# Optimization experiments

Hardware: AMD Instinct MI355X
Metric: run time of the kernel (lower is better)

## Reference

```python
import jax, jax.numpy as jnp
import numpy as np

NODE_DIM = 2
EMB_DIM = 128
SEQ_LEN = 201  # must be odd: depot + N pickups + N deliveries
BATCH = 2048


def _basesin(x, T, fai=0.0):
    return np.sin(2 * np.pi / T * np.abs(np.mod(x, 2 * T) - T) + fai)


def _basecos(x, T, fai=0.0):
    return np.cos(2 * np.pi / T * np.abs(np.mod(x, 2 * T) - T) + fai)


def cyclic_position_encoding_pattern(n_position, emb_dim, mean_pooling=True):
    Td_set = np.linspace(np.power(n_position, 1 / (emb_dim // 2)), n_position,
                         emb_dim // 2, dtype='int')
    x = np.zeros((n_position, emb_dim))
    for i in range(emb_dim):
        Td = Td_set[i // 3 * 3 + 1] if i // 3 * 3 + 1 < emb_dim // 2 else Td_set[-1]
        fai = 0 if i <= emb_dim // 2 else 2 * np.pi * ((-i + emb_dim // 2) / (emb_dim // 2))
        longer = np.arange(0, np.ceil(n_position / Td) * Td, 0.01)
        sel = np.linspace(0, len(longer), n_position, dtype='int', endpoint=False)
        if i % 2 == 1:
            x[:, i] = _basecos(longer, Td, fai)[sel]
        else:
            x[:, i] = _basesin(longer, Td, fai)[sel]
    pattern = x.astype(np.float32)
    pattern_sum = np.zeros_like(pattern)
    arange = np.arange(n_position)
    pooling = [-2, -1, 0, 1, 2] if mean_pooling else [0]
    for i in pooling:
        pattern_sum += pattern[(arange + i + n_position) % n_position]
    pattern = pattern_sum / len(pooling) - pattern.mean(0, keepdims=True)
    return jnp.asarray(pattern)


def setup_inputs() -> dict:
    key = jax.random.key(0)
    kx, kw = jax.random.split(key)
    x = jax.random.normal(kx, (BATCH, SEQ_LEN, NODE_DIM), dtype=jnp.float32)
    # random cyclic permutation per batch: cycle visits all nodes starting at 0
    rng = np.random.default_rng(0)
    r = rng.random((BATCH, SEQ_LEN - 1))
    order = np.concatenate([np.zeros((BATCH, 1), dtype=np.int64),
                            np.argsort(r, axis=1).astype(np.int64) + 1], axis=1)
    nxt = np.roll(order, -1, axis=1)
    sol = np.zeros((BATCH, SEQ_LEN), dtype=np.int64)
    np.put_along_axis(sol, order, nxt, axis=1)
    solutions = jnp.asarray(sol)
    # Linear(node_dim, emb_dim, bias=False), init uniform(-stdv, stdv), stdv=1/sqrt(in)
    stdv = 1.0 / np.sqrt(NODE_DIM)
    W = jax.random.uniform(kw, (EMB_DIM, NODE_DIM), dtype=jnp.float32,
                           minval=-stdv, maxval=stdv)
    pattern = cyclic_position_encoding_pattern(SEQ_LEN, EMB_DIM)
    return {"x": x, "solutions": solutions, "W": W, "pattern": pattern}


def _position_indices(solutions):
    """Pointer-chase over the solution cycle; returns visited_time [B,S] int32
    and top2 [B,S,2] int32 (clac_stacks=True path of the original)."""
    B, S = solutions.shape
    half = S // 2
    arange = jnp.arange(B)
    sol = solutions.astype(jnp.int32)

    visited0 = jnp.zeros((B, S), dtype=jnp.int32)
    pre0 = jnp.zeros((B,), dtype=jnp.int32)
    stacks0 = jnp.full((B, half + 1), -0.01, dtype=jnp.float32).at[:, 0].set(0.0)
    top20 = jnp.zeros((B, S, 2), dtype=jnp.int32)

    def step(carry, i):
        visited, pre, stacks, top2 = carry
        cur = sol[arange, pre]                       # [B] current node
        visited = visited.at[arange, cur].set(i + 1)
        # pickups (0 < cur <= half) push i+1; deliveries (cur > half) pop (-0.01);
        # depot (cur == 0) is a no-op (rewrites stacks[:,0] with itself).
        pos = jnp.where(cur > half, cur - half, cur)
        val = jnp.where(cur == 0, stacks[arange, 0],
                        jnp.where(cur > half, jnp.float32(-0.01),
                                  (i + 1).astype(jnp.float32)))
        stacks = stacks.at[arange, pos].set(val)
        _, idx = jax.lax.top_k(stacks, 2)            # [B,2]
        top2 = top2.at[arange, cur].set(idx.astype(jnp.int32))
        return (visited, cur, stacks, top2), None

    (visited, _, _, top2), _ = jax.lax.scan(
        step, (visited0, pre0, stacks0, top20), jnp.arange(S))
    return visited, top2


def reference(x, solutions, W, pattern):
    visited_time, top2 = _position_indices(solutions)
    S = solutions.shape[1]
    # pos_enc[b, j] = pattern[visited_time[b, j] % S]
    pos_enc = jnp.take(pattern, visited_time % S, axis=0)   # [B,S,D]
    x_embedding = jnp.einsum('bsn,dn->bsd', x, W)           # Linear, no bias
    return x_embedding, pos_enc, visited_time.astype(jnp.int64), top2
```

## Files before the change

kernel.cpp:

```cpp
#include <hip/hip_runtime.h>
#include <stdint.h>

#define B 2048
#define S 201
#define HALF 100
#define D 128
#define BS (B * S)
#define OFF_POS (BS * D)
#define OFF_VT  (2 * OFF_POS)
#define OFF_T2  (OFF_VT + BS)
#define F4B (S * (D / 4))
#define TPB 256

typedef float vf4 __attribute__((ext_vector_type(4)));
typedef float vf2 __attribute__((ext_vector_type(2)));

__global__ __launch_bounds__(TPB, 4) void fused(const float* __restrict__ x,
                                                const int* __restrict__ sol,
                                                const float* __restrict__ W,
                                                const float* __restrict__ pattern,
                                                float* __restrict__ out) {
    __shared__ uint8_t  s_sol[S];
    __shared__ uint8_t  s_vis[S];
    __shared__ uint8_t  s_nx[HALF + 1];
    __shared__ uint8_t  s_pv[HALF + 1];
    __shared__ uint16_t s_t2[S];

    const int tid = threadIdx.x;
    const int b   = blockIdx.x;

    if (tid < 64) {
        for (int j = tid; j < S; j += 64) {
            s_sol[j] = (uint8_t)sol[b * S + j];
            s_vis[j] = 0;
            s_t2[j]  = 0;
        }
        asm volatile("s_waitcnt lgkmcnt(0)" ::: "memory");

        if (tid == 0) {
            int pre = 0;
            int head = 0, second = 1;
            unsigned long long m0 = 0, m1 = 0;

            for (int i = 0; i < S; ++i) {
                int cur = s_sol[pre];
                s_vis[cur] = (uint8_t)(i + 1);
                if (cur != 0) {
                    if (cur <= HALF) {
                        s_nx[cur]  = (uint8_t)head;
                        s_pv[head] = (uint8_t)cur;
                        second = head;
                        head   = cur;
                        if (cur < 64) m0 |= 1ull << cur; else m1 |= 1ull << (cur - 64);
                    } else {
                        int q = cur - HALF;
                        bool in = (q < 64) ? ((m0 >> q) & 1ull)
                                           : ((m1 >> (q - 64)) & 1ull);
                        if (in) {
                            if (q < 64) m0 &= ~(1ull << q); else m1 &= ~(1ull << (q - 64));
                            if (q == head) {
                                head = second;
                                second = (head == 0) ? 1 : (int)s_nx[head];
                            } else if (q == second) {
                                int n2 = s_nx[q];
                                s_nx[head] = (uint8_t)n2;
                                s_pv[n2]   = (uint8_t)head;
                                second = n2;
                            } else {
                                int p = s_pv[q], n2 = s_nx[q];
                                s_nx[p]  = (uint8_t)n2;
                                s_pv[n2] = (uint8_t)p;
                            }
                        }
                    }
                }
                s_t2[cur] = (uint16_t)(head | (second << 8));
                pre = cur;
            }
        }
    } else {
        const int t  = tid - 64;
        const int d4 = t & 31;
        const float4* W4 = (const float4*)W;
        float4 w0 = W4[d4 * 2];
        float4 w1 = W4[d4 * 2 + 1];
        const float2* x2 = (const float2*)x + b * S;
        vf4* o4 = (vf4*)out + b * F4B;
        for (int idx4 = t; idx4 < F4B; idx4 += 192) {
            float2 xv = x2[idx4 >> 5];
            vf4 o;
            o.x = xv.x * w0.x + xv.y * w0.y;
            o.y = xv.x * w0.z + xv.y * w0.w;
            o.z = xv.x * w1.x + xv.y * w1.y;
            o.w = xv.x * w1.z + xv.y * w1.w;
            o4[idx4] = o;
        }
    }
    __syncthreads();

    {
        const vf4* p4 = (const vf4*)pattern;
        vf4* o4 = (vf4*)(out + OFF_POS) + b * F4B;
        for (int idx4 = tid; idx4 < F4B; idx4 += TPB) {
            int vt  = s_vis[idx4 >> 5];
            int row = (vt >= S) ? (vt - S) : vt;
            vf4 v = p4[row * 32 + (idx4 & 31)];
            o4[idx4] = v;
        }
        for (int j = tid; j < S; j += TPB) {
            out[OFF_VT + b * S + j] = (float)s_vis[j];
            int tt = s_t2[j];
            vf2 f2 = { (float)(tt & 255), (float)(tt >> 8) };
            ((vf2*)(out + OFF_T2))[b * S + j] = f2;
        }
    }
}

extern "C" void kernel_launch(void* const* d_in, const int* in_sizes, int n_in,
                              void* d_out, int out_size, void* d_ws, size_t ws_size,
                              hipStream_t stream) {
    const float* x       = (const float*)d_in[0];
    const int*   sol     = (const int*)d_in[1];
    const float* W       = (const float*)d_in[2];
    const float* pattern = (const float*)d_in[3];
    float* out = (float*)d_out;

    hipLaunchKernelGGL(fused, dim3(B), dim3(TPB), 0, stream, x, sol, W, pattern, out);
}
```

Before: 434.1 us.

## Process two batch elements per block with parallel serial chases in two waves

Each block now handles two batch rows, running the serial pointer-chasing stack simulation for both at once in separate wavefronts (lanes 0 and 64), while the other two waves write the linear embedding for both rows. The grid is halved. The aim is to overlap two latency-bound serial chains per block and amortise block launch and setup. The cost is fewer embedding-writing threads per row, a barrier now shared by both rows, and half as many blocks to hide latency.

Result: slower. 454.4 us (+4.7%).

```diff
diff --git a/kernel.cpp b/kernel.cpp
--- a/kernel.cpp
+++ b/kernel.cpp
@@ -11,105 +11,120 @@
 #define OFF_T2  (OFF_VT + BS)
 #define F4B (S * (D / 4))
 #define TPB 256
+#define NBLK (B / 2)
 
 typedef float vf4 __attribute__((ext_vector_type(4)));
 typedef float vf2 __attribute__((ext_vector_type(2)));
+
+__device__ __forceinline__ void chase(const uint8_t* __restrict__ sl,
+                                      uint8_t* __restrict__ vis,
+                                      uint16_t* __restrict__ t2,
+                                      uint8_t* __restrict__ nx,
+                                      uint8_t* __restrict__ pv) {
+    int pre = 0;
+    int head = 0, second = 1;
+    unsigned long long m0 = 0, m1 = 0;
+    for (int i = 0; i < S; ++i) {
+        int cur = sl[pre];
+        vis[cur] = (uint8_t)(i + 1);
+        if (cur != 0) {
+            if (cur <= HALF) {
+                nx[cur]  = (uint8_t)head;
+                pv[head] = (uint8_t)cur;
+                second = head;
+                head   = cur;
+                if (cur < 64) m0 |= 1ull << cur; else m1 |= 1ull << (cur - 64);
+            } else {
+                int q = cur - HALF;
+                bool in = (q < 64) ? ((m0 >> q) & 1ull) : ((m1 >> (q - 64)) & 1ull);
+                if (in) {
+                    if (q < 64) m0 &= ~(1ull << q); else m1 &= ~(1ull << (q - 64));
+                    if (q == head) {
+                        head = second;
+                        second = (head == 0) ? 1 : (int)nx[head];
+                    } else if (q == second) {
+                        int n2 = nx[q];
+                        nx[head] = (uint8_t)n2;
+                        pv[n2]   = (uint8_t)head;
+                        second = n2;
+                    } else {
+                        int p = pv[q], n2 = nx[q];
+                        nx[p]  = (uint8_t)n2;
+                        pv[n2] = (uint8_t)p;
+                    }
+                }
+            }
+        }
+        t2[cur] = (uint16_t)(head | (second << 8));
+        pre = cur;
+    }
+}
 
 __global__ __launch_bounds__(TPB, 4) void fused(const float* __restrict__ x,
                                                 const int* __restrict__ sol,
                                                 const float* __restrict__ W,
                                                 const float* __restrict__ pattern,
                                                 float* __restrict__ out) {
-    __shared__ uint8_t  s_sol[S];
-    __shared__ uint8_t  s_vis[S];
-    __shared__ uint8_t  s_nx[HALF + 1];
-    __shared__ uint8_t  s_pv[HALF + 1];
-    __shared__ uint16_t s_t2[S];
+    __shared__ uint8_t  s_sol[2][S];
+    __shared__ uint8_t  s_vis[2][S];
+    __shared__ uint16_t s_t2 [2][S];
+    __shared__ uint8_t  s_nx [2][HALF + 1];
+    __shared__ uint8_t  s_pv [2][HALF + 1];
 
     const int tid = threadIdx.x;
-    const int b   = blockIdx.x;
+    const int b0  = blockIdx.x;
+    const int b1  = blockIdx.x + NBLK;
 
-    if (tid < 64) {
-        for (int j = tid; j < S; j += 64) {
-            s_sol[j] = (uint8_t)sol[b * S + j];
-            s_vis[j] = 0;
-            s_t2[j]  = 0;
-        }
-        asm volatile("s_waitcnt lgkmcnt(0)" ::: "memory");
+    for (int j = tid; j < S; j += TPB) {
+        s_sol[0][j] = (uint8_t)sol[b0 * S + j];
+        s_sol[1][j] = (uint8_t)sol[b1 * S + j];
+        s_vis[0][j] = 0;  s_vis[1][j] = 0;
+        s_t2 [0][j] = 0;  s_t2 [1][j] = 0;
+    }
+    __syncthreads();
 
-        if (tid == 0) {
-            int pre = 0;
-            int head = 0, second = 1;
-            unsigned long long m0 = 0, m1 = 0;
-
-            for (int i = 0; i < S; ++i) {
-                int cur = s_sol[pre];
-                s_vis[cur] = (uint8_t)(i + 1);
-                if (cur != 0) {
-                    if (cur <= HALF) {
-                        s_nx[cur]  = (uint8_t)head;
-                        s_pv[head] = (uint8_t)cur;
-                        second = head;
-                        head   = cur;
-                        if (cur < 64) m0 |= 1ull << cur; else m1 |= 1ull << (cur - 64);
-                    } else {
-                        int q = cur - HALF;
-                        bool in = (q < 64) ? ((m0 >> q) & 1ull)
-                                           : ((m1 >> (q - 64)) & 1ull);
-                        if (in) {
-                            if (q < 64) m0 &= ~(1ull << q); else m1 &= ~(1ull << (q - 64));
-                            if (q == head) {
-                                head = second;
-                                second = (head == 0) ? 1 : (int)s_nx[head];
-                            } else if (q == second) {
-                                int n2 = s_nx[q];
-                                s_nx[head] = (uint8_t)n2;
-                                s_pv[n2]   = (uint8_t)head;
-                                second = n2;
-                            } else {
-                                int p = s_pv[q], n2 = s_nx[q];
-                                s_nx[p]  = (uint8_t)n2;
-                                s_pv[n2] = (uint8_t)p;
-                            }
-                        }
-                    }
-                }
-                s_t2[cur] = (uint16_t)(head | (second << 8));
-                pre = cur;
-            }
+    if (tid < 128) {
+        if ((tid & 63) == 0) {
+            const int w = tid >> 6;
+            chase(s_sol[w], s_vis[w], s_t2[w], s_nx[w], s_pv[w]);
         }
     } else {
-        const int t  = tid - 64;
+        const int t  = tid - 128;
         const int d4 = t & 31;
         const float4* W4 = (const float4*)W;
         float4 w0 = W4[d4 * 2];
         float4 w1 = W4[d4 * 2 + 1];
-        const float2* x2 = (const float2*)x + b * S;
-        vf4* o4 = (vf4*)out + b * F4B;
-        for (int idx4 = t; idx4 < F4B; idx4 += 192) {
-            float2 xv = x2[idx4 >> 5];
-            vf4 o;
-            o.x = xv.x * w0.x + xv.y * w0.y;
-            o.y = xv.x * w0.z + xv.y * w0.w;
-            o.z = xv.x * w1.x + xv.y * w1.y;
-            o.w = xv.x * w1.z + xv.y * w1.w;
-            o4[idx4] = o;
+        #pragma unroll
+        for (int h = 0; h < 2; ++h) {
+            const int b = h ? b1 : b0;
+            const float2* x2 = (const float2*)x + b * S;
+            vf4* o4 = (vf4*)out + b * F4B;
+            for (int idx4 = t; idx4 < F4B; idx4 += 128) {
+                float2 xv = x2[idx4 >> 5];
+                vf4 o;
+                o.x = xv.x * w0.x + xv.y * w0.y;
+                o.y = xv.x * w0.z + xv.y * w0.w;
+                o.z = xv.x * w1.x + xv.y * w1.y;
+                o.w = xv.x * w1.z + xv.y * w1.w;
+                o4[idx4] = o;
+            }
         }
     }
     __syncthreads();
 
-    {
-        const vf4* p4 = (const vf4*)pattern;
+    const vf4* p4 = (const vf4*)pattern;
+    #pragma unroll
+    for (int h = 0; h < 2; ++h) {
+        const int b = h ? b1 : b0;
         vf4* o4 = (vf4*)(out + OFF_POS) + b * F4B;
         for (int idx4 = tid; idx4 < F4B; idx4 += TPB) {
-            int vt  = s_vis[idx4 >> 5];
+            int vt  = s_vis[h][idx4 >> 5];
             int row = (vt >= S) ? (vt - S) : vt;
-            vf4 v = p4[row * 32 + (idx4 & 31)];
-            o4[idx4] = v;
+            o4[idx4] = p4[row * 32 + (idx4 & 31)];
         }
         for (int j = tid; j < S; j += TPB) {
-            out[OFF_VT + b * S + j] = (float)s_vis[j];
-            int tt = s_t2[j];
+            out[OFF_VT + b * S + j] = (float)s_vis[h][j];
+            int tt = s_t2[h][j];
             vf2 f2 = { (float)(tt & 255), (float)(tt >> 8) };
             ((vf2*)(out + OFF_T2))[b * S + j] = f2;
         }
@@ -125,5 +140,5 @@
     const float* pattern = (const float*)d_in[3];
     float* out = (float*)d_out;
 
-    hipLaunchKernelGGL(fused, dim3(B), dim3(TPB), 0, stream, x, sol, W, pattern, out);
+    hipLaunchKernelGGL(fused, dim3(NBLK), dim3(TPB), 0, stream, x, sol, W, pattern, out);
 }
```

## Replace serial linked-list stack tracking with parallel per-node top-2 scan

Applied to the files above, without the earlier changes.

The single-thread serial walk now records only visit times. Each node's top-2 stack entries are then recomputed in parallel: one thread per node scans all 100 pickup/delivery pairs using the visit times to decide which pickups are still open at that moment. This removes the branchy linked-list bookkeeping from the serial critical path, at the cost of about 100 shared-memory reads per node per thread. Launch bounds are also raised to 8 blocks per CU.

Measured after the change: 439.3 us. Within noise of the previous version (+1.2%).

```diff
diff --git a/kernel.cpp b/kernel.cpp
--- a/kernel.cpp
+++ b/kernel.cpp
@@ -15,66 +15,27 @@
 typedef float vf4 __attribute__((ext_vector_type(4)));
 typedef float vf2 __attribute__((ext_vector_type(2)));
 
-__global__ __launch_bounds__(TPB, 4) void fused(const float* __restrict__ x,
+__global__ __launch_bounds__(TPB, 8) void fused(const float* __restrict__ x,
                                                 const int* __restrict__ sol,
                                                 const float* __restrict__ W,
                                                 const float* __restrict__ pattern,
                                                 float* __restrict__ out) {
-    __shared__ uint8_t  s_sol[S];
-    __shared__ uint8_t  s_vis[S];
-    __shared__ uint8_t  s_nx[HALF + 1];
-    __shared__ uint8_t  s_pv[HALF + 1];
-    __shared__ uint16_t s_t2[S];
+    __shared__ uint8_t s_sol[S];
+    __shared__ uint8_t s_vis[S];
 
     const int tid = threadIdx.x;
     const int b   = blockIdx.x;
 
     if (tid < 64) {
-        for (int j = tid; j < S; j += 64) {
+        for (int j = tid; j < S; j += 64)
             s_sol[j] = (uint8_t)sol[b * S + j];
-            s_vis[j] = 0;
-            s_t2[j]  = 0;
-        }
         asm volatile("s_waitcnt lgkmcnt(0)" ::: "memory");
-
         if (tid == 0) {
             int pre = 0;
-            int head = 0, second = 1;
-            unsigned long long m0 = 0, m1 = 0;
-
+            #pragma unroll 1
             for (int i = 0; i < S; ++i) {
                 int cur = s_sol[pre];
                 s_vis[cur] = (uint8_t)(i + 1);
-                if (cur != 0) {
-                    if (cur <= HALF) {
-                        s_nx[cur]  = (uint8_t)head;
-                        s_pv[head] = (uint8_t)cur;
-                        second = head;
-                        head   = cur;
-                        if (cur < 64) m0 |= 1ull << cur; else m1 |= 1ull << (cur - 64);
-                    } else {
-                        int q = cur - HALF;
-                        bool in = (q < 64) ? ((m0 >> q) & 1ull)
-                                           : ((m1 >> (q - 64)) & 1ull);
-                        if (in) {
-                            if (q < 64) m0 &= ~(1ull << q); else m1 &= ~(1ull << (q - 64));
-                            if (q == head) {
-                                head = second;
-                                second = (head == 0) ? 1 : (int)s_nx[head];
-                            } else if (q == second) {
-                                int n2 = s_nx[q];
-                                s_nx[head] = (uint8_t)n2;
-                                s_pv[n2]   = (uint8_t)head;
-                                second = n2;
-                            } else {
-                                int p = s_pv[q], n2 = s_nx[q];
-                                s_nx[p]  = (uint8_t)n2;
-                                s_pv[n2] = (uint8_t)p;
-                            }
-                        }
-                    }
-                }
-                s_t2[cur] = (uint16_t)(head | (second << 8));
                 pre = cur;
             }
         }
@@ -98,20 +59,30 @@
     }
     __syncthreads();
 
+    for (int c = tid; c < S; c += TPB) {
+        int t = s_vis[c];
+        int best = 0, bi = 0, sec = -1, si = 1;
+        #pragma unroll 4
+        for (int q = 1; q <= HALF; ++q) {
+            int vp = s_vis[q];
+            int vd = s_vis[q + HALF];
+            bool open = (vp <= t) && !((vp < vd) && (vd <= t));
+            int v = open ? vp : -1;
+            if (v > best) { sec = best; si = bi; best = v; bi = q; }
+            else if (v > sec) { sec = v; si = q; }
+        }
+        out[OFF_VT + b * S + c] = (float)t;
+        vf2 f2 = { (float)bi, (float)si };
+        ((vf2*)(out + OFF_T2))[b * S + c] = f2;
+    }
+
     {
         const vf4* p4 = (const vf4*)pattern;
         vf4* o4 = (vf4*)(out + OFF_POS) + b * F4B;
         for (int idx4 = tid; idx4 < F4B; idx4 += TPB) {
             int vt  = s_vis[idx4 >> 5];
             int row = (vt >= S) ? (vt - S) : vt;
-            vf4 v = p4[row * 32 + (idx4 & 31)];
-            o4[idx4] = v;
-        }
-        for (int j = tid; j < S; j += TPB) {
-            out[OFF_VT + b * S + j] = (float)s_vis[j];
-            int tt = s_t2[j];
-            vf2 f2 = { (float)(tt & 255), (float)(tt >> 8) };
-            ((vf2*)(out + OFF_T2))[b * S + j] = f2;
+            o4[idx4] = p4[row * 32 + (idx4 & 31)];
         }
     }
 }
```
